# Kernel tuning notes

Measured on AMD Instinct MI355X. Metric: run time of the kernel, lower is better.

Reference implementation:

```python
import jax, jax.numpy as jnp
import numpy as np

B, T, D, H = 2, 2048, 1024, 16
HD = D // H
ALPHA = HD ** -0.5
EPS = 1e-5


def setup_inputs() -> dict:
    key = jax.random.key(0)
    ks = jax.random.split(key, 8)
    x = jax.random.normal(ks[0], (B, T, D), dtype=jnp.float32)
    # additive causal mask: 0 where allowed, -inf where disallowed
    causal = jnp.triu(jnp.ones((T, T), dtype=bool), k=1)
    attention_mask = jnp.where(causal, -jnp.inf, 0.0).astype(jnp.float32)
    rab = jax.random.normal(ks[1], (1, H, T, T), dtype=jnp.float32) * 0.02
    W_in = jax.random.normal(ks[2], (D, 4 * D), dtype=jnp.float32) * (D ** -0.5)
    b_in = jnp.zeros((4 * D,), dtype=jnp.float32)
    W_out = jax.random.normal(ks[3], (D, D), dtype=jnp.float32) * (D ** -0.5)
    b_out = jnp.zeros((D,), dtype=jnp.float32)
    ln_w = jnp.ones((D,), dtype=jnp.float32)
    ln_b = jnp.zeros((D,), dtype=jnp.float32)
    return {"x": x, "attention_mask": attention_mask, "rab": rab,
            "W_in": W_in, "b_in": b_in, "W_out": W_out, "b_out": b_out,
            "ln_w": ln_w, "ln_b": ln_b}


def _heads(t):  # [B,T,D] -> [B,H,T,HD]
    return t.reshape(B, T, H, HD).transpose(0, 2, 1, 3)


def _layernorm(t, w, b):
    mu = jnp.mean(t, axis=-1, keepdims=True)
    var = jnp.mean(jnp.square(t - mu), axis=-1, keepdims=True)
    return (t - mu) * jax.lax.rsqrt(var + EPS) * w + b


def reference(x, attention_mask, rab, W_in, b_in, W_out, b_out, ln_w, ln_b):
    h = jax.nn.silu(x @ W_in + b_in)                      # [B,T,4D]
    U, V, Q, K = jnp.split(h, 4, axis=-1)
    Qh, Kh, Vh = _heads(Q), _heads(K), _heads(V)
    logits = jnp.einsum('bhqd,bhkd->bhqk', Qh, Kh) * ALPHA
    logits = logits + rab + attention_mask[None, None]    # [B,H,T,T]
    # allowed counts from the additive mask (0 == allowed)
    allowed = (attention_mask == 0).astype(jnp.float32)   # [T,T]
    denom = jnp.clip(jnp.sum(allowed, axis=-1, keepdims=True), 1.0)  # [T,1]
    logits_safe = jnp.where(jnp.isinf(logits) & (logits < 0), -1e9, logits)
    attn = jax.nn.silu(logits_safe) / denom[None, None]
    AV = jnp.einsum('bhqk,bhkd->bhqd', attn, Vh)
    AV = AV.transpose(0, 2, 1, 3).reshape(B, T, D)
    y = (_layernorm(AV, ln_w, ln_b) * U) @ W_out + b_out
    return y
```

## Files before the change

### kernel.cpp

```cpp
#include <hip/hip_runtime.h>

#define BATCH 2
#define TSEQ 2048
#define DIM 1024
#define NH 16
#define HDIM 64
#define MROWS (BATCH * TSEQ)

typedef __attribute__((ext_vector_type(4))) float f32x4;
typedef __attribute__((ext_vector_type(8))) short short8;

__device__ __forceinline__ unsigned short f2bf(float f) {
    union { float f; unsigned int u; } x; x.f = f;
    unsigned int r = x.u + 0x7fffu + ((x.u >> 16) & 1u);
    return (unsigned short)(r >> 16);
}

__device__ __forceinline__ float silu_f(float v) {
    return v * __builtin_amdgcn_rcpf(1.f + __expf(-v));
}

__device__ __forceinline__ void gl_lds16(const void* g, void* l) {
    __builtin_amdgcn_global_load_lds(
        (const __attribute__((address_space(1))) void*)g,
        (__attribute__((address_space(3))) void*)l, 16, 0, 0);
}

__device__ __forceinline__ short8 rd_swz(const unsigned short* base, int row, int chunk) {
    const char* b = (const char*)base;
    return *(const short8*)(b + row * 128 + (((chunk ^ (row & 7)) << 4)));
}

__global__ __launch_bounds__(256) void k_convert(const float* __restrict__ in,
                                                 unsigned short* __restrict__ out,
                                                 int n4) {
    int i = blockIdx.x * 256 + threadIdx.x;
    if (i < n4) {
        float4 v = ((const float4*)in)[i];
        union { unsigned short s[4]; uint2 u; } o;
        o.s[0] = f2bf(v.x); o.s[1] = f2bf(v.y); o.s[2] = f2bf(v.z); o.s[3] = f2bf(v.w);
        ((uint2*)out)[i] = o.u;
    }
}

__global__ __launch_bounds__(256) void k_transpose(const float* __restrict__ in,
                                                   unsigned short* __restrict__ out,
                                                   int R, int C) {
    __shared__ float tile[32][33];
    int tx = threadIdx.x, ty = threadIdx.y;
    int c0 = blockIdx.x * 32, r0 = blockIdx.y * 32;
    #pragma unroll
    for (int i = 0; i < 32; i += 8)
        tile[ty + i][tx] = in[(size_t)(r0 + ty + i) * C + c0 + tx];
    __syncthreads();
    #pragma unroll
    for (int i = 0; i < 32; i += 8)
        out[(size_t)(c0 + ty + i) * R + r0 + tx] = f2bf(tile[tx][ty + i]);
}

__device__ __forceinline__ void stage256(const unsigned short* __restrict__ A,
                                         const unsigned short* __restrict__ Bt,
                                         int row0, int col0, int k0,
                                         unsigned short* sAbuf, unsigned short* sBbuf,
                                         int tid) {
    #pragma unroll
    for (int q = 0; q < 4; ++q) {
        int c = tid + 512 * q;
        int rr = c >> 3;
        int kcs = (c & 7) ^ (rr & 7);
        gl_lds16(A + (size_t)(row0 + rr) * 1024 + k0 + kcs * 8, sAbuf + c * 8);
        gl_lds16(Bt + (size_t)(col0 + rr) * 1024 + k0 + kcs * 8, sBbuf + c * 8);
    }
}

__global__ __launch_bounds__(512, 2) void k_gemm1_256(
    const unsigned short* __restrict__ A, const unsigned short* __restrict__ Bt,
    const float* __restrict__ bias,
    float* __restrict__ outU, unsigned short* __restrict__ outVt,
    unsigned short* __restrict__ outQ, unsigned short* __restrict__ outK)
{
    __shared__ __align__(16) unsigned short sA[2][256 * 64];
    __shared__ __align__(16) unsigned short sB[2][256 * 64];

    const int tid = threadIdx.x;
    const int lane = tid & 63, wid = tid >> 6;
    const int lr = lane & 15, lk = lane >> 4;
    const int wm = wid >> 2, wn = wid & 3;
    const int bm = blockIdx.x, bn = blockIdx.y;
    const int row0 = bm * 256, col0 = bn * 256;

    f32x4 acc[8][4] = {};

    stage256(A, Bt, row0, col0, 0, sA[0], sB[0], tid);
    asm volatile("s_waitcnt vmcnt(0)" ::: "memory");
    __builtin_amdgcn_s_barrier();
    __builtin_amdgcn_sched_barrier(0);

    int cur = 0;
    for (int kt = 0; kt < 16; ++kt) {
        if (kt < 15) stage256(A, Bt, row0, col0, (kt + 1) * 64, sA[cur ^ 1], sB[cur ^ 1], tid);
        short8 bf[2][4];
        #pragma unroll
        for (int kk = 0; kk < 2; ++kk)
            #pragma unroll
            for (int n = 0; n < 4; ++n)
                bf[kk][n] = rd_swz(sB[cur], wn * 64 + n * 16 + lr, kk * 4 + lk);

        #pragma unroll
        for (int ph = 0; ph < 4; ++ph) {
            short8 af[2][2];
            #pragma unroll
            for (int mm = 0; mm < 2; ++mm)
                #pragma unroll
                for (int kk = 0; kk < 2; ++kk)
                    af[mm][kk] = rd_swz(sA[cur], wm * 128 + (ph * 2 + mm) * 16 + lr, kk * 4 + lk);
            __builtin_amdgcn_s_barrier();
            __builtin_amdgcn_s_setprio(1);
            #pragma unroll
            for (int mm = 0; mm < 2; ++mm)
                #pragma unroll
                for (int n = 0; n < 4; ++n)
                    #pragma unroll
                    for (int kk = 0; kk < 2; ++kk)
                        acc[ph * 2 + mm][n] = __builtin_amdgcn_mfma_f32_16x16x32_bf16(
                            af[mm][kk], bf[kk][n], acc[ph * 2 + mm][n], 0, 0, 0);
            __builtin_amdgcn_s_setprio(0);
            if (ph == 3) asm volatile("s_waitcnt vmcnt(0)" ::: "memory");
            __builtin_amdgcn_s_barrier();
        }
        __builtin_amdgcn_sched_barrier(0);
        cur ^= 1;
    }

    const int sec = bn >> 2;
    #pragma unroll
    for (int n = 0; n < 4; ++n) {
        const int cg = col0 + wn * 64 + n * 16 + lr;
        const int cc = cg & 1023;
        const float bv = bias[cg];
        #pragma unroll
        for (int m = 0; m < 8; ++m) {
            const int rg0 = row0 + wm * 128 + m * 16 + lk * 4;
            float sv[4];
            #pragma unroll
            for (int j = 0; j < 4; ++j)
                sv[j] = silu_f(acc[m][n][j] + bv);
            if (sec == 0) {
                #pragma unroll
                for (int j = 0; j < 4; ++j)
                    outU[((size_t)(rg0 + j) << 10) + cc] = sv[j];
            } else if (sec == 1) {
                union { unsigned short s[4]; uint2 u; } pk;
                #pragma unroll
                for (int j = 0; j < 4; ++j) pk.s[j] = f2bf(sv[j]);
                *(uint2*)(outVt + ((size_t)cc << 12) + rg0) = pk.u;
            } else if (sec == 2) {
                #pragma unroll
                for (int j = 0; j < 4; ++j)
                    outQ[((size_t)(rg0 + j) << 10) + cc] = f2bf(sv[j] * 0.125f);
            } else {
                #pragma unroll
                for (int j = 0; j < 4; ++j)
                    outK[((size_t)(rg0 + j) << 10) + cc] = f2bf(sv[j]);
            }
        }
    }
}

__global__ __launch_bounds__(256) void k_gemm2(
    const unsigned short* __restrict__ A, const unsigned short* __restrict__ Bt,
    int M, int N, int K, const float* __restrict__ bias, float* __restrict__ outY)
{
    __shared__ __align__(16) unsigned short sA[128 * 32];
    __shared__ __align__(16) unsigned short sB[128 * 32];
    const int tid = threadIdx.x;
    const int bm = blockIdx.x, bn = blockIdx.y;
    const int row0 = bm * 128, col0 = bn * 128;
    const int lane = tid & 63, w = tid >> 6;
    const int wrow = (w >> 1) * 64, wcol = (w & 1) * 64;
    const int lr = lane & 15, lk = lane >> 4;

    f32x4 acc[4][4] = {};

    for (int k0 = 0; k0 < K; k0 += 32) {
        for (int c = tid; c < 512; c += 256) {
            int r = c >> 2, kc = c & 3;
            gl_lds16(A + (size_t)(row0 + r) * K + k0 + kc * 8, sA + c * 8);
            gl_lds16(Bt + (size_t)(col0 + r) * K + k0 + kc * 8, sB + c * 8);
        }
        __syncthreads();
        short8 af[4], bf[4];
        #pragma unroll
        for (int m = 0; m < 4; ++m)
            af[m] = *(const short8*)(sA + (wrow + m * 16 + lr) * 32 + lk * 8);
        #pragma unroll
        for (int n = 0; n < 4; ++n)
            bf[n] = *(const short8*)(sB + (wcol + n * 16 + lr) * 32 + lk * 8);
        #pragma unroll
        for (int m = 0; m < 4; ++m)
            #pragma unroll
            for (int n = 0; n < 4; ++n)
                acc[m][n] = __builtin_amdgcn_mfma_f32_16x16x32_bf16(af[m], bf[n], acc[m][n], 0, 0, 0);
        __syncthreads();
    }

    #pragma unroll
    for (int m = 0; m < 4; ++m) {
        #pragma unroll
        for (int n = 0; n < 4; ++n) {
            int cg = col0 + wcol + n * 16 + lr;
            float bv = bias[cg];
            int rg0 = row0 + wrow + m * 16 + lk * 4;
            #pragma unroll
            for (int j = 0; j < 4; ++j)
                outY[(size_t)(rg0 + j) * N + cg] = acc[m][n][j] + bv;
        }
    }
}

__global__ __launch_bounds__(256, 4) void k_attn(
    const unsigned short* __restrict__ Qb,
    const unsigned short* __restrict__ Kb,
    const unsigned short* __restrict__ Vt,
    const float* __restrict__ rab,
    float* __restrict__ AV)
{
    __shared__ __align__(16) unsigned short sK[2][64 * 64];
    __shared__ __align__(16) unsigned short sVt[2][64 * 64];
    __shared__ __align__(16) unsigned short sP[64 * 64];

    const int tid = threadIdx.x;
    const int lane = tid & 63;
    const int w = tid >> 6;
    const int lr = lane & 15;
    const int lk = lane >> 4;

    const int bid = blockIdx.x;
    const int idx = bid & 255;
    const int g = bid >> 8;
    const int h = idx & 15;
    const int r_ = idx >> 4;
    const int bb = g >> 1;
    const int qt = (g & 1) ? (31 - r_) : r_;
    const int q0 = qt * 64;

    short8 qreg[2];
    #pragma unroll
    for (int ks = 0; ks < 2; ++ks)
        qreg[ks] = *(const short8*)(Qb + (((size_t)(bb * TSEQ + q0 + w * 16 + lr)) << 10)
                                     + h * 64 + ks * 32 + lk * 8);

    int qrow[4];
    const float* rabrow[4];
    const float* rabh = rab + (size_t)h * TSEQ * TSEQ;
    #pragma unroll
    for (int j = 0; j < 4; ++j) {
        qrow[j] = q0 + w * 16 + lk * 4 + j;
        rabrow[j] = rabh + (size_t)qrow[j] * TSEQ + lr;
    }

    f32x4 acc[4] = {};

    #define STAGE(buf, kt_) do {                                                      \
        int k0s = (kt_) * 64;                                                         \
        for (int c = tid; c < 512; c += 256) {                                        \
            int rr = c >> 3, kc = c & 7;                                              \
            int kcs = kc ^ (rr & 7);                                                  \
            gl_lds16(Kb + (((size_t)(bb * TSEQ + k0s + rr)) << 10) + h * 64 + kcs * 8,\
                     sK[buf] + c * 8);                                                \
            gl_lds16(Vt + (((size_t)(h * 64 + rr)) << 12) + bb * TSEQ + k0s + kcs * 8,\
                     sVt[buf] + c * 8);                                               \
        }                                                                             \
    } while (0)

    STAGE(0, 0);
    float rvc[4][4];
    #pragma unroll
    for (int nt = 0; nt < 4; ++nt)
        #pragma unroll
        for (int j = 0; j < 4; ++j)
            rvc[nt][j] = rabrow[j][nt * 16];
    __syncthreads();

    int cur = 0;
    for (int kt = 0; kt <= qt; ++kt) {
        const int k0 = kt * 64;
        const bool have_next = (kt < qt);
        if (have_next) STAGE(cur ^ 1, kt + 1);

        float rvn[4][4];
        if (have_next) {
            #pragma unroll
            for (int nt = 0; nt < 4; ++nt)
                #pragma unroll
                for (int j = 0; j < 4; ++j)
                    rvn[nt][j] = rabrow[j][k0 + 64 + nt * 16];
        }

        f32x4 s[4];
        #pragma unroll
        for (int nt = 0; nt < 4; ++nt) {
            f32x4 c0v;
            c0v[0] = rvc[nt][0]; c0v[1] = rvc[nt][1];
            c0v[2] = rvc[nt][2]; c0v[3] = rvc[nt][3];
            s[nt] = c0v;
        }
        #pragma unroll
        for (int ks = 0; ks < 2; ++ks) {
            #pragma unroll
            for (int nt = 0; nt < 4; ++nt)
                s[nt] = __builtin_amdgcn_mfma_f32_16x16x32_bf16(
                    qreg[ks], rd_swz(sK[cur], nt * 16 + lr, ks * 4 + lk), s[nt], 0, 0, 0);
        }

        const bool full = (kt < qt);
        char* pb = (char*)sP;
        #pragma unroll
        for (int j = 0; j < 4; ++j) {
            const int prow = w * 16 + lk * 4 + j;
            char* bj = pb + prow * 128;
            const int swz = ((lk * 4 + j) & 7) << 4;
            #pragma unroll
            for (int nt = 0; nt < 4; ++nt) {
                int k = k0 + nt * 16 + lr;
                float pv = (full || k <= qrow[j]) ? silu_f(s[nt][j]) : 0.f;
                *(unsigned short*)(bj + (((nt << 5) | (lr << 1)) ^ swz)) = f2bf(pv);
            }
        }

        #pragma unroll
        for (int ks = 0; ks < 2; ++ks) {
            short8 ap = rd_swz(sP, w * 16 + lr, ks * 4 + lk);
            #pragma unroll
            for (int dt = 0; dt < 4; ++dt)
                acc[dt] = __builtin_amdgcn_mfma_f32_16x16x32_bf16(
                    ap, rd_swz(sVt[cur], dt * 16 + lr, ks * 4 + lk), acc[dt], 0, 0, 0);
        }

        if (have_next) {
            #pragma unroll
            for (int nt = 0; nt < 4; ++nt)
                #pragma unroll
                for (int j = 0; j < 4; ++j)
                    rvc[nt][j] = rvn[nt][j];
        }

        __syncthreads();
        cur ^= 1;
    }
    #undef STAGE

    #pragma unroll
    for (int dt = 0; dt < 4; ++dt)
        #pragma unroll
        for (int j = 0; j < 4; ++j)
            AV[(((size_t)(bb * TSEQ + qrow[j])) << 10) + h * 64 + dt * 16 + lr] = acc[dt][j];
}

__global__ __launch_bounds__(256) void k_ln(const float* __restrict__ AV,
                                            const float* __restrict__ U,
                                            const float* __restrict__ lnw,
                                            const float* __restrict__ lnb,
                                            unsigned short* __restrict__ z) {
    __shared__ float red[8];
    const int row = blockIdx.x, tid = threadIdx.x;
    const float c = (float)((row & (TSEQ - 1)) + 1);
    const float eps = 1e-5f * c * c;
    float4 v = ((const float4*)(AV + ((size_t)row << 10)))[tid];
    float s = v.x + v.y + v.z + v.w;
    float s2 = v.x * v.x + v.y * v.y + v.z * v.z + v.w * v.w;
    #pragma unroll
    for (int o = 32; o > 0; o >>= 1) { s += __shfl_xor(s, o); s2 += __shfl_xor(s2, o); }
    const int w = tid >> 6;
    if ((tid & 63) == 0) { red[w] = s; red[4 + w] = s2; }
    __syncthreads();
    s = red[0] + red[1] + red[2] + red[3];
    s2 = red[4] + red[5] + red[6] + red[7];
    const float mu = s * (1.f / 1024.f);
    const float var = s2 * (1.f / 1024.f) - mu * mu;
    const float rstd = rsqrtf(var + eps);
    float4 uw = ((const float4*)(U + ((size_t)row << 10)))[tid];
    float4 lw = ((const float4*)lnw)[tid];
    float4 lb = ((const float4*)lnb)[tid];
    union { unsigned short o[4]; uint2 u; } ov;
    ov.o[0] = f2bf(((v.x - mu) * rstd * lw.x + lb.x) * uw.x);
    ov.o[1] = f2bf(((v.y - mu) * rstd * lw.y + lb.y) * uw.y);
    ov.o[2] = f2bf(((v.z - mu) * rstd * lw.z + lb.z) * uw.z);
    ov.o[3] = f2bf(((v.w - mu) * rstd * lw.w + lb.w) * uw.w);
    ((uint2*)z)[((size_t)row << 8) + tid] = ov.u;
}

extern "C" void kernel_launch(void* const* d_in, const int* in_sizes, int n_in,
                              void* d_out, int out_size, void* d_ws, size_t ws_size,
                              hipStream_t stream) {
    const float* x     = (const float*)d_in[0];
    const float* rab   = (const float*)d_in[2];
    const float* W_in  = (const float*)d_in[3];
    const float* b_in  = (const float*)d_in[4];
    const float* W_out = (const float*)d_in[5];
    const float* b_out = (const float*)d_in[6];
    const float* ln_w  = (const float*)d_in[7];
    const float* ln_b  = (const float*)d_in[8];
    float* y = (float*)d_out;

    char* ws = (char*)d_ws;
    size_t off = 0;
    auto alloc = [&](size_t bytes) -> void* {
        void* p = ws + off;
        off += (bytes + 255) & ~(size_t)255;
        return p;
    };
    unsigned short* WinT  = (unsigned short*)alloc((size_t)4096 * 1024 * 2);
    unsigned short* WoutT = (unsigned short*)alloc((size_t)1024 * 1024 * 2);
    unsigned short* xb    = (unsigned short*)alloc((size_t)MROWS * DIM * 2);
    float*          Ubuf  = (float*)alloc((size_t)MROWS * DIM * 4);
    unsigned short* Qb    = (unsigned short*)alloc((size_t)MROWS * DIM * 2);
    unsigned short* Kb    = (unsigned short*)alloc((size_t)MROWS * DIM * 2);
    unsigned short* Vtb   = (unsigned short*)alloc((size_t)DIM * MROWS * 2);
    float*          AV    = (float*)alloc((size_t)MROWS * DIM * 4);
    unsigned short* z     = (unsigned short*)alloc((size_t)MROWS * DIM * 2);

    k_convert<<<dim3(4096), dim3(256), 0, stream>>>(x, xb, MROWS * DIM / 4);
    k_transpose<<<dim3(128, 32), dim3(32, 8), 0, stream>>>(W_in, WinT, 1024, 4096);
    k_transpose<<<dim3(32, 32), dim3(32, 8), 0, stream>>>(W_out, WoutT, 1024, 1024);
    k_gemm1_256<<<dim3(16, 16), dim3(512), 0, stream>>>(xb, WinT, b_in, Ubuf, Vtb, Qb, Kb);
    k_attn<<<dim3(1024), dim3(256), 0, stream>>>(Qb, Kb, Vtb, rab, AV);
    k_ln<<<dim3(MROWS), dim3(256), 0, stream>>>(AV, Ubuf, ln_w, ln_b, z);
    k_gemm2<<<dim3(32, 8), dim3(256), 0, stream>>>(z, WoutT, MROWS, 1024, 1024, b_out, y);
}
```

Measured before the change: 173.2 us.

## Unroll attention loop by two with ping-pong rab registers and partial vmcnt waits

Unrolls the causal attention K-tile loop by two so the prefetched rab values alternate between two register arrays instead of being copied each iteration. The full-barrier sync is replaced by an explicit `s_waitcnt vmcnt(16)` plus `s_barrier`, which waits only for the K/V LDS staging loads and leaves the rab prefetch loads in flight across the barrier. The mask check is split so only the diagonal tile does the causal compare. Scheduling barriers pin instruction order; the change relies on the exact count of outstanding loads per thread, which is fragile if the staging pattern changes.

```diff
diff --git a/kernel.cpp b/kernel.cpp
--- a/kernel.cpp
+++ b/kernel.cpp
@@ -249,6 +249,7 @@
     for (int ks = 0; ks < 2; ++ks)
         qreg[ks] = *(const short8*)(Qb + (((size_t)(bb * TSEQ + q0 + w * 16 + lr)) << 10)
                                      + h * 64 + ks * 32 + lk * 8);
+    __builtin_amdgcn_sched_barrier(0);
 
     int qrow[4];
     const float* rabrow[4];
@@ -273,81 +274,92 @@
         }                                                                             \
     } while (0)
 
+    float rv0[4][4], rv1[4][4];
+
     STAGE(0, 0);
-    float rvc[4][4];
+    __builtin_amdgcn_sched_barrier(0);
     #pragma unroll
     for (int nt = 0; nt < 4; ++nt)
         #pragma unroll
         for (int j = 0; j < 4; ++j)
-            rvc[nt][j] = rabrow[j][nt * 16];
-    __syncthreads();
-
-    int cur = 0;
-    for (int kt = 0; kt <= qt; ++kt) {
-        const int k0 = kt * 64;
-        const bool have_next = (kt < qt);
-        if (have_next) STAGE(cur ^ 1, kt + 1);
-
-        float rvn[4][4];
-        if (have_next) {
-            #pragma unroll
-            for (int nt = 0; nt < 4; ++nt)
-                #pragma unroll
-                for (int j = 0; j < 4; ++j)
-                    rvn[nt][j] = rabrow[j][k0 + 64 + nt * 16];
-        }
-
-        f32x4 s[4];
-        #pragma unroll
-        for (int nt = 0; nt < 4; ++nt) {
-            f32x4 c0v;
-            c0v[0] = rvc[nt][0]; c0v[1] = rvc[nt][1];
-            c0v[2] = rvc[nt][2]; c0v[3] = rvc[nt][3];
-            s[nt] = c0v;
-        }
-        #pragma unroll
-        for (int ks = 0; ks < 2; ++ks) {
-            #pragma unroll
-            for (int nt = 0; nt < 4; ++nt)
-                s[nt] = __builtin_amdgcn_mfma_f32_16x16x32_bf16(
-                    qreg[ks], rd_swz(sK[cur], nt * 16 + lr, ks * 4 + lk), s[nt], 0, 0, 0);
-        }
-
-        const bool full = (kt < qt);
-        char* pb = (char*)sP;
-        #pragma unroll
-        for (int j = 0; j < 4; ++j) {
-            const int prow = w * 16 + lk * 4 + j;
-            char* bj = pb + prow * 128;
-            const int swz = ((lk * 4 + j) & 7) << 4;
-            #pragma unroll
-            for (int nt = 0; nt < 4; ++nt) {
-                int k = k0 + nt * 16 + lr;
-                float pv = (full || k <= qrow[j]) ? silu_f(s[nt][j]) : 0.f;
-                *(unsigned short*)(bj + (((nt << 5) | (lr << 1)) ^ swz)) = f2bf(pv);
-            }
-        }
-
-        #pragma unroll
-        for (int ks = 0; ks < 2; ++ks) {
-            short8 ap = rd_swz(sP, w * 16 + lr, ks * 4 + lk);
-            #pragma unroll
-            for (int dt = 0; dt < 4; ++dt)
-                acc[dt] = __builtin_amdgcn_mfma_f32_16x16x32_bf16(
-                    ap, rd_swz(sVt[cur], dt * 16 + lr, ks * 4 + lk), acc[dt], 0, 0, 0);
-        }
-
-        if (have_next) {
-            #pragma unroll
-            for (int nt = 0; nt < 4; ++nt)
-                #pragma unroll
-                for (int j = 0; j < 4; ++j)
-                    rvc[nt][j] = rvn[nt][j];
-        }
-
-        __syncthreads();
-        cur ^= 1;
-    }
+            rv0[nt][j] = rabrow[j][nt * 16];
+    __builtin_amdgcn_sched_barrier(0);
+    asm volatile("s_waitcnt vmcnt(16)" ::: "memory");
+    __builtin_amdgcn_s_barrier();
+
+    #define BODY(KT, BUFC, RVC, RVN) do {                                             \
+        const int k0 = (KT) * 64;                                                     \
+        const bool have_next = (KT) < qt;                                             \
+        if (have_next) STAGE((BUFC) ^ 1, (KT) + 1);                                   \
+        __builtin_amdgcn_sched_barrier(0);                                            \
+        if (have_next) {                                                              \
+            _Pragma("unroll")                                                         \
+            for (int nt = 0; nt < 4; ++nt)                                            \
+                _Pragma("unroll")                                                     \
+                for (int j = 0; j < 4; ++j)                                           \
+                    RVN[nt][j] = rabrow[j][k0 + 64 + nt * 16];                        \
+        }                                                                             \
+        __builtin_amdgcn_sched_barrier(0);                                            \
+        f32x4 s[4];                                                                   \
+        _Pragma("unroll")                                                             \
+        for (int nt = 0; nt < 4; ++nt) {                                              \
+            f32x4 c0v;                                                                \
+            c0v[0] = RVC[nt][0]; c0v[1] = RVC[nt][1];                                 \
+            c0v[2] = RVC[nt][2]; c0v[3] = RVC[nt][3];                                 \
+            s[nt] = c0v;                                                              \
+        }                                                                             \
+        _Pragma("unroll")                                                             \
+        for (int ks = 0; ks < 2; ++ks) {                                              \
+            _Pragma("unroll")                                                         \
+            for (int nt = 0; nt < 4; ++nt)                                            \
+                s[nt] = __builtin_amdgcn_mfma_f32_16x16x32_bf16(                      \
+                    qreg[ks], rd_swz(sK[BUFC], nt * 16 + lr, ks * 4 + lk), s[nt], 0, 0, 0); \
+        }                                                                             \
+        char* pb = (char*)sP;                                                         \
+        if (have_next) {                                                              \
+            _Pragma("unroll")                                                         \
+            for (int j = 0; j < 4; ++j) {                                             \
+                const int prow = w * 16 + lk * 4 + j;                                 \
+                char* bj = pb + prow * 128;                                           \
+                const int swz = ((lk * 4 + j) & 7) << 4;                              \
+                _Pragma("unroll")                                                     \
+                for (int nt = 0; nt < 4; ++nt)                                        \
+                    *(unsigned short*)(bj + (((nt << 5) | (lr << 1)) ^ swz))          \
+                        = f2bf(silu_f(s[nt][j]));                                     \
+            }                                                                         \
+        } else {                                                                      \
+            _Pragma("unroll")                                                         \
+            for (int j = 0; j < 4; ++j) {                                             \
+                const int prow = w * 16 + lk * 4 + j;                                 \
+                char* bj = pb + prow * 128;                                           \
+                const int swz = ((lk * 4 + j) & 7) << 4;                              \
+                _Pragma("unroll")                                                     \
+                for (int nt = 0; nt < 4; ++nt) {                                      \
+                    int k = k0 + nt * 16 + lr;                                        \
+                    float pv = (k <= qrow[j]) ? silu_f(s[nt][j]) : 0.f;               \
+                    *(unsigned short*)(bj + (((nt << 5) | (lr << 1)) ^ swz)) = f2bf(pv); \
+                }                                                                     \
+            }                                                                         \
+        }                                                                             \
+        _Pragma("unroll")                                                             \
+        for (int ks = 0; ks < 2; ++ks) {                                              \
+            short8 ap = rd_swz(sP, w * 16 + lr, ks * 4 + lk);                         \
+            _Pragma("unroll")                                                         \
+            for (int dt = 0; dt < 4; ++dt)                                            \
+                acc[dt] = __builtin_amdgcn_mfma_f32_16x16x32_bf16(                    \
+                    ap, rd_swz(sVt[BUFC], dt * 16 + lr, ks * 4 + lk), acc[dt], 0, 0, 0); \
+        }                                                                             \
+        if (have_next) {                                                              \
+            asm volatile("s_waitcnt vmcnt(16)" ::: "memory");                         \
+            __builtin_amdgcn_s_barrier();                                             \
+        }                                                                             \
+    } while (0)
+
+    for (int kt = 0; kt <= qt; kt += 2) {
+        BODY(kt, 0, rv0, rv1);
+        if (kt + 1 <= qt) BODY(kt + 1, 1, rv1, rv0);
+    }
+    #undef BODY
     #undef STAGE
 
     #pragma unroll
```

New measurement: 170.7 us. Within noise of the previous version (-1.4%).
